# Kernel optimization log

Measured on AMD Instinct MI355X. Metric: run time of the kernel, lower is better.

Reference implementation:

```python
import jax, jax.numpy as jnp
import numpy as np

# config constants (match init_kwargs)
C = 1024
NH = 16
HS = C // NH
CHUNK = 64          # attn_chunk_size
TOPK = 32           # attn_topk
WINDOW = 4096       # kv_cache_window_size
MIN_KV = 16384      # min_kv_cache_size
MAX_KV = 32768      # max_kv_cache_size
SHORT = 4096        # short_sequence_criteria
CT = 65536          # incoming kv-cache length


def setup_inputs() -> dict:
    key = jax.random.key(0)
    ks = jax.random.split(key, 7)
    s = 1.0 / np.sqrt(C)
    return {
        "x": jax.random.normal(ks[0], (C,), jnp.float32),
        "k_cache": jax.random.normal(ks[1], (1, CT, C), jnp.float32),
        "v_cache": jax.random.normal(ks[2], (1, CT, C), jnp.float32),
        "Wr": jax.random.normal(ks[3], (C, C), jnp.float32) * s,
        "Wk": jax.random.normal(ks[4], (C, C), jnp.float32) * s,
        "Wv": jax.random.normal(ks[5], (C, C), jnp.float32) * s,
        "Wo": jax.random.normal(ks[6], (C, C), jnp.float32) * s,
    }


def _split_heads(t):  # (1, T, C) -> (1, NH, T, HS)
    return t.reshape(1, t.shape[1], NH, HS).transpose(0, 2, 1, 3)


def _update_kv_cache(q, k_cache, v_cache):
    # q: (1,1,C); caches: (1,CT,C). CT > MIN_KV so compression runs.
    past = CT - WINDOW
    kp = _split_heads(k_cache[:, :past])          # (1,NH,past,HS)
    vp = _split_heads(v_cache[:, :past])
    qh = _split_heads(q)                          # (1,NH,1,HS)
    scores = jnp.einsum("bhqd,bhkd->bhqk", qh, kp) / np.sqrt(HS)
    w = jax.nn.softmax(scores, axis=-1)           # (1,NH,1,past)
    vote = w.sum(axis=-2)                         # (1,NH,past)
    keep = MIN_KV - WINDOW                        # per-head tokens kept
    _, idx = jax.lax.top_k(vote, keep)            # (1,NH,keep), descending vote order
    kpc = jnp.take_along_axis(kp, idx[..., None], axis=2)  # (1,NH,keep,HS)
    vpc = jnp.take_along_axis(vp, idx[..., None], axis=2)
    kpc = kpc.transpose(0, 2, 1, 3).reshape(1, keep, C)
    vpc = vpc.transpose(0, 2, 1, 3).reshape(1, keep, C)
    k_new = jnp.concatenate([kpc, k_cache[:, past:]], axis=1)  # (1, MIN_KV, C)
    v_new = jnp.concatenate([vpc, v_cache[:, past:]], axis=1)
    return k_new, v_new


def reference(x, k_cache, v_cache, Wr, Wk, Wv, Wo):
    x2 = x[None, None, :]                         # (1,1,C)
    q = x2 @ Wr.T
    k = x2 @ Wk.T
    v = x2 @ Wv.T

    # CT > MAX_KV -> compress cache (eviction via attention vote per head)
    k_cache, v_cache = _update_kv_cache(q, k_cache, v_cache)
    CT2 = k_cache.shape[1]                        # MIN_KV = 16384 > SHORT -> sparse path

    num_chunks = CT2 // CHUNK
    kc = k_cache.reshape(1, num_chunks, CHUNK, C)
    vc = v_cache.reshape(1, num_chunks, CHUNK, C)
    chunk_key = kc.mean(axis=2)                   # (1,num_chunks,C)
    chunk_score = jnp.einsum("bqc,bkc->bqk", q, chunk_key)
    _, tidx = jax.lax.top_k(chunk_score[0, 0], TOPK)  # (TOPK,)
    topk_k = kc[:, tidx].reshape(1, TOPK * CHUNK, C)
    topk_v = vc[:, tidx].reshape(1, TOPK * CHUNK, C)

    k_comb = jnp.concatenate([topk_k, k], axis=1)  # (1, TOPK*CHUNK+1, C)
    v_comb = jnp.concatenate([topk_v, v], axis=1)

    qh = _split_heads(q)                          # (1,NH,1,HS)
    kh = _split_heads(k_comb)
    vh = _split_heads(v_comb)
    attn = jax.nn.softmax(
        jnp.einsum("bhqd,bhkd->bhqk", qh, kh) / np.sqrt(HS), axis=-1)
    y = jnp.einsum("bhqk,bhkd->bhqd", attn, vh)   # (1,NH,1,HS)
    y = y.transpose(0, 2, 1, 3).reshape(C)
    y = y @ Wo.T
    return y
```

## Files before the change

kernel.cpp:

```cpp
#include <hip/hip_runtime.h>
#include <stdint.h>

#define C      1024
#define NH     16
#define HS     64
#define CT     65536
#define PAST   61440
#define KEEP   12288
#define NCOMP  192
#define NSEL   32
#define NB     8192
#define NBLK   256

typedef unsigned long long ull;

#define LD_A(p)   __hip_atomic_load((p), __ATOMIC_RELAXED, __HIP_MEMORY_SCOPE_AGENT)
#define ST_A(p,v) __hip_atomic_store((p), (v), __ATOMIC_RELAXED, __HIP_MEMORY_SCOPE_AGENT)

__device__ __forceinline__ unsigned int desc_key(float f) {
    unsigned int b = __float_as_uint(f);
    return (b >> 31) ? b : (~b & 0x7FFFFFFFu);
}
__device__ __forceinline__ float u_to_f(unsigned int u) {
    unsigned int b = (u & 0x80000000u) ? u : (0x7FFFFFFFu - u);
    return __uint_as_float(b);
}
__device__ __forceinline__ int bin_of(float s, float hi, float scale) {
    int b = (int)((hi - s) * scale);
    return b < 0 ? 0 : (b > NB - 1 ? NB - 1 : b);
}
__device__ __forceinline__ void load_params(const unsigned* umin, const unsigned* umax,
                                            int h, float* hi, float* sc) {
    float h2 = u_to_f(umin[h]);
    float lo = u_to_f(umax[h]);
    float r = h2 - lo;
    *hi = h2;
    *sc = (r > 0.f) ? (float)(NB - 1) / r : 0.f;
}

#define GRPW 32
#define SITEW 288
__device__ __forceinline__ void gsync(unsigned* bar, int site) {
    __syncthreads();
    if (threadIdx.x == 0) {
        asm volatile("s_waitcnt vmcnt(0)" ::: "memory");
        unsigned* g    = bar + site * SITEW + (blockIdx.x >> 5) * GRPW;
        unsigned* root = bar + site * SITEW + 8 * GRPW;
        if (__hip_atomic_fetch_add(g, 1u, __ATOMIC_RELAXED, __HIP_MEMORY_SCOPE_AGENT) == 31u)
            __hip_atomic_fetch_add(root, 1u, __ATOMIC_RELAXED, __HIP_MEMORY_SCOPE_AGENT);
        while (LD_A(root) < 8u) __builtin_amdgcn_s_sleep(16);
    }
    __syncthreads();
}

__global__ void k_proj(const float* __restrict__ x, const float* __restrict__ Wr,
                       const float* __restrict__ Wk, const float* __restrict__ Wv,
                       float* __restrict__ q, float* __restrict__ kn, float* __restrict__ vn,
                       unsigned* __restrict__ hist, unsigned* __restrict__ umin,
                       unsigned* __restrict__ umax, ull* __restrict__ cs_fix,
                       unsigned* __restrict__ bar) {
    int id = blockIdx.x * 256 + threadIdx.x;
    if (id < NH * NB) hist[id] = 0;
    if (blockIdx.x >= 512 && blockIdx.x < 520)
        bar[(blockIdx.x - 512) * 256 + threadIdx.x] = 0u;
    if (blockIdx.x == 700) {
        if (threadIdx.x < 16) umin[threadIdx.x] = 0xFFFFFFFFu;
        else if (threadIdx.x < 32) umax[threadIdx.x - 16] = 0u;
    }
    if (blockIdx.x == 701 && threadIdx.x < 256) cs_fix[threadIdx.x] = 0ull;

    int w = blockIdx.x * (blockDim.x >> 6) + (threadIdx.x >> 6);
    int lane = threadIdx.x & 63;
    int mat = w >> 10, row = w & 1023;
    const float* W = (mat == 0) ? Wr : (mat == 1) ? Wk : Wv;
    const float4* Wrow = (const float4*)(W + (size_t)row * C);
    const float4* x4 = (const float4*)x;
    float acc = 0.f;
#pragma unroll
    for (int i = 0; i < 4; ++i) {
        float4 a = Wrow[i * 64 + lane];
        float4 b = x4[i * 64 + lane];
        acc += a.x * b.x + a.y * b.y + a.z * b.z + a.w * b.w;
    }
#pragma unroll
    for (int off = 32; off; off >>= 1) acc += __shfl_xor(acc, off);
    if (lane == 0) { (mat == 0 ? q : (mat == 1 ? kn : vn))[row] = acc; }
}

__global__ void k_scores(const float* __restrict__ kc, const float* __restrict__ q,
                         float* __restrict__ s, unsigned* __restrict__ umin,
                         unsigned* __restrict__ umax) {
    __shared__ float sc_l[4][16][17];
    __shared__ float smn[4][16], smx[4][16];
    int wave = threadIdx.x >> 6, lane = threadIdx.x & 63;
    int wid = blockIdx.x * 4 + wave;
    int t0 = wid * 16;
    const float4* q4 = (const float4*)q;
    float4 qv[4];
#pragma unroll
    for (int i = 0; i < 4; ++i) qv[i] = q4[i * 64 + lane];
    float mnv[4] = {3.4e38f, 3.4e38f, 3.4e38f, 3.4e38f};
    float mxv[4] = {-3.4e38f, -3.4e38f, -3.4e38f, -3.4e38f};
    for (int tt = 0; tt < 16; ++tt) {
        const float4* row = (const float4*)(kc + (size_t)(t0 + tt) * C);
        float acc[4];
#pragma unroll
        for (int i = 0; i < 4; ++i) {
            float4 a = row[i * 64 + lane];
            acc[i] = a.x * qv[i].x + a.y * qv[i].y + a.z * qv[i].z + a.w * qv[i].w;
        }
#pragma unroll
        for (int off = 8; off; off >>= 1) {
#pragma unroll
            for (int i = 0; i < 4; ++i) acc[i] += __shfl_xor(acc[i], off);
        }
        if ((lane & 15) == 0) {
            int g = lane >> 4;
#pragma unroll
            for (int i = 0; i < 4; ++i) {
                sc_l[wave][4 * i + g][tt] = acc[i];
                mnv[i] = fminf(mnv[i], acc[i]);
                mxv[i] = fmaxf(mxv[i], acc[i]);
            }
        }
    }
    __syncthreads();
    int tt2 = lane & 15;
#pragma unroll
    for (int r = 0; r < 4; ++r) {
        int h = r * 4 + (lane >> 4);
        s[(size_t)h * CT + t0 + tt2] = sc_l[wave][h][tt2];
    }
    if (blockIdx.x < 960) {
        if ((lane & 15) == 0) {
            int g = lane >> 4;
#pragma unroll
            for (int i = 0; i < 4; ++i) { smn[wave][4 * i + g] = mnv[i]; smx[wave][4 * i + g] = mxv[i]; }
        }
        __syncthreads();
        if (threadIdx.x < 16) {
            int h = threadIdx.x;
            float mn = smn[0][h], mx = smx[0][h];
            for (int w2 = 1; w2 < 4; ++w2) {
                mn = fminf(mn, smn[w2][h]);
                mx = fmaxf(mx, smx[w2][h]);
            }
            atomicMin(&umin[h], desc_key(mx));
            atomicMax(&umax[h], desc_key(mn));
        }
    }
}

__global__ __launch_bounds__(1024, 2) void k_mega(
        const float* __restrict__ s, const float* __restrict__ vc,
        const unsigned* __restrict__ umin, const unsigned* __restrict__ umax,
        unsigned* __restrict__ base, unsigned* __restrict__ Tarr,
        ull* __restrict__ G, unsigned* __restrict__ stok,
        ull* __restrict__ cs_fix, float* __restrict__ part,
        const float* __restrict__ q, const float* __restrict__ kn,
        const float* __restrict__ vn, const float* __restrict__ Wo,
        float* __restrict__ out, unsigned* __restrict__ bar) {
    const int bid = blockIdx.x, tid = threadIdx.x;
    const int lane = tid & 63, wave = tid >> 6;
    __shared__ __align__(16) char smem[40960];
    __shared__ unsigned tarr_l[16];
    __shared__ unsigned shT, shN;

    {
        unsigned* lh = (unsigned*)smem;
        int h = bid >> 4, seg = bid & 15;
        for (int i = tid; i < NB; i += 1024) lh[i] = 0;
        __syncthreads();
        float hi, sc; load_params(umin, umax, h, &hi, &sc);
        const float* sh = s + (size_t)h * CT + seg * 3840;
        for (int i = tid; i < 3840; i += 1024)
            atomicAdd(&lh[bin_of(sh[i], hi, sc)], 1u);
        __syncthreads();
        unsigned* gh = base + h * NB;
        for (int i = tid; i < NB; i += 1024) {
            unsigned c = lh[i];
            if (c) atomicAdd(&gh[i], c);
        }
    }
    gsync(bar, 0);

    if (bid < 16) {
        unsigned* wsum = (unsigned*)smem;
        unsigned* B = base + bid * NB;
        unsigned cnt[8];
        unsigned loc = 0;
        int b0 = tid * 8;
#pragma unroll
        for (int k = 0; k < 8; ++k) { cnt[k] = LD_A(&B[b0 + k]); loc += cnt[k]; }
        unsigned run = loc;
#pragma unroll
        for (int off = 1; off < 64; off <<= 1) {
            unsigned n = __shfl_up(run, off);
            if (lane >= off) run += n;
        }
        if (lane == 63) wsum[wave] = run;
        __syncthreads();
        if (wave == 0 && lane < 16) {
            unsigned v = wsum[lane];
#pragma unroll
            for (int off = 1; off < 16; off <<= 1) {
                unsigned n = __shfl_up(v, off);
                if (lane >= off) v += n;
            }
            wsum[lane] = v;
        }
        __syncthreads();
        unsigned r = run - loc + (wave ? wsum[wave - 1] : 0u);
#pragma unroll
        for (int k = 0; k < 8; ++k) {
            unsigned c = cnt[k];
            ST_A(&B[b0 + k], r);
            unsigned inc = r + c;
            if (r < KEEP && inc >= KEEP) ST_A(&Tarr[bid], (unsigned)(b0 + k));
            r = inc;
        }
    } else {
        int gw = (bid - 16) * 16 + wave;
        if (gw < NH * 64) {
            int h = gw >> 6, c2 = gw & 63;
            float v = s[(size_t)h * CT + PAST + c2 * 64 + lane];
            long long f = llrintf(v * 16777216.f);
#pragma unroll
            for (int off = 32; off; off >>= 1) f += __shfl_xor(f, off);
            if (lane == 0) atomicAdd(&cs_fix[NCOMP + c2], (ull)f);
        }
    }
    gsync(bar, 1);

    if (tid < 16) tarr_l[tid] = LD_A(&Tarr[tid]);
    __syncthreads();
    for (int i = bid * 1024 + tid; i < NH * PAST; i += NBLK * 1024) {
        int h = i / PAST, t = i - h * PAST;
        float hi, sc; load_params(umin, umax, h, &hi, &sc);
        float v = s[(size_t)h * CT + t];
        int b = bin_of(v, hi, sc);
        if ((unsigned)b <= tarr_l[h]) {
            unsigned pos = atomicAdd(&base[h * NB + b], 1u);
            ST_A(&G[(size_t)h * 65536 + pos], ((ull)desc_key(v) << 16) | (unsigned)t);
        }
    }
    gsync(bar, 2);

    {
        ull* csl = (ull*)smem;
        if (tid < NCOMP) csl[tid] = 0ull;
        int h = bid >> 4, seg = bid & 15;
        if (tid == 0) {
            unsigned T = LD_A(&Tarr[h]);
            shT = T;
            shN = LD_A(&base[h * NB + T]);
        }
        __syncthreads();
        float hi, sc; load_params(umin, umax, h, &hi, &sc);
        unsigned ncand = shN;
        const ull* Gh = G + (size_t)h * 65536;
        for (unsigned p = seg * 1024 + tid; p < ncand; p += 16384) {
            ull pk = Gh[p];
            unsigned u = (unsigned)(pk >> 16);
            float v = u_to_f(u);
            int b = bin_of(v, hi, sc);
            unsigned start = b ? LD_A(&base[h * NB + b - 1]) : 0u;
            unsigned end = LD_A(&base[h * NB + b]);
            unsigned rank = start;
            for (unsigned j = start; j < end; ++j) rank += (Gh[j] < pk) ? 1u : 0u;
            if (rank < KEEP) {
                ST_A(&stok[h * KEEP + rank], (unsigned)(pk & 0xFFFFull));
                long long f = llrintf(v * 16777216.f);
                atomicAdd(&csl[rank >> 6], (ull)f);
            }
        }
        __syncthreads();
        if (tid < NCOMP) {
            ull c = csl[tid];
            if (c) atomicAdd(&cs_fix[tid], c);
        }
    }
    gsync(bar, 3);

    {
        ull* key = (ull*)smem;
        unsigned* sel_l = (unsigned*)(smem + 2048);
        float* scm = (float*)(smem + 2176);
        float* exb = (float*)(smem + 2688);
        float* vbuf = (float*)(smem + 3200);
        if (tid < 256) {
            long long v = (long long)cs_fix[tid];
            ull bb = (ull)(v + (1ll << 45));
            key[tid] = (((1ull << 46) - bb) << 8) | (unsigned)tid;
        }
        __syncthreads();
        for (unsigned k = 2; k <= 256; k <<= 1) {
            for (unsigned j = k >> 1; j > 0; j >>= 1) {
                if (tid < 256) {
                    unsigned ixj = tid ^ j;
                    if (ixj > (unsigned)tid) {
                        ull a = key[tid], b = key[ixj];
                        bool up = ((tid & k) == 0);
                        if (up ? (a > b) : (a < b)) { key[tid] = b; key[ixj] = a; }
                    }
                }
                __syncthreads();
            }
        }
        if (tid < NSEL) sel_l[tid] = (unsigned)(key[tid] & 0xFFull);
        __syncthreads();

        int su = tid >> 9, sid = tid & 511;
        int p = bid * 2 + su;
        int h = p >> 5, ci = p & 31;
        int c = (int)sel_l[ci];
        int g = sid >> 3, q8 = sid & 7;
        int t = (c < NCOMP) ? (int)stok[h * KEEP + c * 64 + g]
                            : (PAST + (c - NCOMP) * 64 + g);
        if (q8 == 0) scm[su * 64 + g] = s[(size_t)h * CT + t] * 0.125f;
        __syncthreads();
        float m = -1e30f;
        for (int j = 0; j < 64; ++j) m = fmaxf(m, scm[su * 64 + j]);
        float e = expf(scm[su * 64 + g] - m);
        if (q8 == 0) exb[su * 64 + g] = e;
        const float4* vrow = (const float4*)(vc + (size_t)t * C + h * HS);
        float4 v0 = vrow[q8 * 2], v1 = vrow[q8 * 2 + 1];
        float* vb = vbuf + su * 4352 + g * 68 + q8 * 8;
        vb[0] = e * v0.x; vb[1] = e * v0.y; vb[2] = e * v0.z; vb[3] = e * v0.w;
        vb[4] = e * v1.x; vb[5] = e * v1.y; vb[6] = e * v1.z; vb[7] = e * v1.w;
        __syncthreads();
        if (sid < 64) {
            float acc = 0.f;
            for (int g2 = 0; g2 < 64; ++g2) acc += vbuf[su * 4352 + g2 * 68 + sid];
            float* P = part + (size_t)(h * 32 + ci) * 68;
            ST_A(&P[2 + sid], acc);
            if (sid == 0) {
                float es = 0.f;
                for (int g2 = 0; g2 < 64; ++g2) es += exb[su * 64 + g2];
                ST_A(&P[0], m);
                ST_A(&P[1], es);
            }
        }
    }
    gsync(bar, 4);
    if (bid >= 64) return;

    {
        float* yl = (float*)smem;
        float* qdl = (float*)(smem + 4096);
        if (tid < 16) {
            float qd = 0.f;
            for (int l = 0; l < 64; ++l) qd += q[tid * 64 + l] * kn[tid * 64 + l];
            qdl[tid] = qd;
        }
        __syncthreads();
        {
            int h = tid >> 6, ln = tid & 63;
            float a_new = qdl[h] * 0.125f;
            const float* P0 = part + (size_t)h * 32 * 68;
            float m = a_new;
            for (int ci = 0; ci < 32; ++ci) m = fmaxf(m, P0[ci * 68]);
            float den = expf(a_new - m);
            float acc = den * vn[h * HS + ln];
            for (int ci = 0; ci < 32; ++ci) {
                float w = expf(P0[ci * 68] - m);
                den += w * P0[ci * 68 + 1];
                acc += w * P0[ci * 68 + 2 + ln];
            }
            yl[tid] = acc / den;
        }
        __syncthreads();
        int r = bid * 16 + wave;
        const float4* Wrow = (const float4*)(Wo + (size_t)r * C);
        const float4* y4 = (const float4*)yl;
        float acc = 0.f;
#pragma unroll
        for (int i = 0; i < 4; ++i) {
            float4 a = Wrow[i * 64 + lane];
            float4 b = y4[i * 64 + lane];
            acc += a.x * b.x + a.y * b.y + a.z * b.z + a.w * b.w;
        }
#pragma unroll
        for (int off = 32; off; off >>= 1) acc += __shfl_xor(acc, off);
        if (lane == 0) out[r] = acc;
    }
}

extern "C" void kernel_launch(void* const* d_in, const int* in_sizes, int n_in,
                              void* d_out, int out_size, void* d_ws, size_t ws_size,
                              hipStream_t stream) {
    const float* x  = (const float*)d_in[0];
    const float* kc = (const float*)d_in[1];
    const float* vc = (const float*)d_in[2];
    const float* Wr = (const float*)d_in[3];
    const float* Wk = (const float*)d_in[4];
    const float* Wv = (const float*)d_in[5];
    const float* Wo = (const float*)d_in[6];
    float* out = (float*)d_out;
    char* ws = (char*)d_ws;

    float* q    = (float*)(ws + 0);
    float* kn   = (float*)(ws + 8192);
    float* vn   = (float*)(ws + 16384);
    ull* cs_fix = (ull*)(ws + 32768);
    float* part = (float*)(ws + 49152);
    unsigned* stok = (unsigned*)(ws + 196608);
    unsigned* umin = (unsigned*)(ws + 1048576);
    unsigned* umax = (unsigned*)(ws + 1048640);
    unsigned* Tarr = (unsigned*)(ws + 1048704);
    unsigned* bar  = (unsigned*)(ws + 1048832);
    unsigned* base = (unsigned*)(ws + 1114112);
    float* s = (float*)(ws + 2097152);
    ull* G = (ull*)(ws + 6291456);

    k_proj<<<768, 256, 0, stream>>>(x, Wr, Wk, Wv, q, kn, vn, base, umin, umax, cs_fix, bar);
    k_scores<<<1024, 256, 0, stream>>>(kc, q, s, umin, umax);
    k_mega<<<NBLK, 1024, 0, stream>>>(s, vc, umin, umax, base, Tarr, G, stok, cs_fix,
                                      part, q, kn, vn, Wo, out, bar);
}
```

Measured before the change: 143.4 us.

## Replace grid-wide barriers with per-head barriers and local histogram scans

Histogram building, prefix scan, and candidate scatter now happen per head among that head's 16 blocks, synchronised by a per-head counter barrier instead of three grid-wide barriers. Each block redoes the head's prefix scan in shared memory, and scatters from its own segment using a separate count array. The window-chunk fixed-point sum moves into k_scores' otherwise idle tail blocks. The aim is to cut global barrier latency and serial phases at the cost of redundant scans and more workspace zeroing.

Result: faster. 130.4 us (-9.0%).

```diff
diff --git a/kernel.cpp b/kernel.cpp
--- a/kernel.cpp
+++ b/kernel.cpp
@@ -38,29 +38,37 @@
     *sc = (r > 0.f) ? (float)(NB - 1) / r : 0.f;
 }
 
-#define GRPW 32
-#define SITEW 288
 __device__ __forceinline__ void gsync(unsigned* bar, int site) {
     __syncthreads();
     if (threadIdx.x == 0) {
         asm volatile("s_waitcnt vmcnt(0)" ::: "memory");
-        unsigned* g    = bar + site * SITEW + (blockIdx.x >> 5) * GRPW;
-        unsigned* root = bar + site * SITEW + 8 * GRPW;
+        unsigned* g    = bar + site * 288 + (blockIdx.x >> 5) * 32;
+        unsigned* root = bar + site * 288 + 256;
         if (__hip_atomic_fetch_add(g, 1u, __ATOMIC_RELAXED, __HIP_MEMORY_SCOPE_AGENT) == 31u)
             __hip_atomic_fetch_add(root, 1u, __ATOMIC_RELAXED, __HIP_MEMORY_SCOPE_AGENT);
         while (LD_A(root) < 8u) __builtin_amdgcn_s_sleep(16);
     }
     __syncthreads();
 }
+__device__ __forceinline__ void hsync(unsigned* bar, int site, int h) {
+    __syncthreads();
+    if (threadIdx.x == 0) {
+        asm volatile("s_waitcnt vmcnt(0)" ::: "memory");
+        unsigned* c = bar + 576 + (site * 16 + h) * 32;
+        __hip_atomic_fetch_add(c, 1u, __ATOMIC_RELAXED, __HIP_MEMORY_SCOPE_AGENT);
+        while (LD_A(c) < 16u) __builtin_amdgcn_s_sleep(8);
+    }
+    __syncthreads();
+}
 
 __global__ void k_proj(const float* __restrict__ x, const float* __restrict__ Wr,
                        const float* __restrict__ Wk, const float* __restrict__ Wv,
                        float* __restrict__ q, float* __restrict__ kn, float* __restrict__ vn,
-                       unsigned* __restrict__ hist, unsigned* __restrict__ umin,
+                       unsigned* __restrict__ hc, unsigned* __restrict__ umin,
                        unsigned* __restrict__ umax, ull* __restrict__ cs_fix,
                        unsigned* __restrict__ bar) {
-    int id = blockIdx.x * 256 + threadIdx.x;
-    if (id < NH * NB) hist[id] = 0;
+    int gid = blockIdx.x * 256 + threadIdx.x;
+    for (int i = gid; i < 2 * NH * NB; i += 196608) hc[i] = 0;
     if (blockIdx.x >= 512 && blockIdx.x < 520)
         bar[(blockIdx.x - 512) * 256 + threadIdx.x] = 0u;
     if (blockIdx.x == 700) {
@@ -89,9 +97,10 @@
 
 __global__ void k_scores(const float* __restrict__ kc, const float* __restrict__ q,
                          float* __restrict__ s, unsigned* __restrict__ umin,
-                         unsigned* __restrict__ umax) {
+                         unsigned* __restrict__ umax, ull* __restrict__ cs_fix) {
     __shared__ float sc_l[4][16][17];
     __shared__ float smn[4][16], smx[4][16];
+    __shared__ long long wred[4];
     int wave = threadIdx.x >> 6, lane = threadIdx.x & 63;
     int wid = blockIdx.x * 4 + wave;
     int t0 = wid * 16;
@@ -148,13 +157,25 @@
             atomicMin(&umin[h], desc_key(mx));
             atomicMax(&umax[h], desc_key(mn));
         }
+    } else {
+        int hh = threadIdx.x >> 4, tt = threadIdx.x & 15;
+        long long f = 0;
+#pragma unroll
+        for (int w2 = 0; w2 < 4; ++w2) f += llrintf(sc_l[w2][hh][tt] * 16777216.f);
+#pragma unroll
+        for (int off = 32; off; off >>= 1) f += __shfl_xor(f, off);
+        if (lane == 0) wred[wave] = f;
+        __syncthreads();
+        if (threadIdx.x == 0)
+            cs_fix[NCOMP + (blockIdx.x - 960)] =
+                (ull)(wred[0] + wred[1] + wred[2] + wred[3]);
     }
 }
 
 __global__ __launch_bounds__(1024, 2) void k_mega(
         const float* __restrict__ s, const float* __restrict__ vc,
         const unsigned* __restrict__ umin, const unsigned* __restrict__ umax,
-        unsigned* __restrict__ base, unsigned* __restrict__ Tarr,
+        unsigned* __restrict__ hist, unsigned* __restrict__ cnt,
         ull* __restrict__ G, unsigned* __restrict__ stok,
         ull* __restrict__ cs_fix, float* __restrict__ part,
         const float* __restrict__ q, const float* __restrict__ kn,
@@ -162,36 +183,34 @@
         float* __restrict__ out, unsigned* __restrict__ bar) {
     const int bid = blockIdx.x, tid = threadIdx.x;
     const int lane = tid & 63, wave = tid >> 6;
+    const int h = bid >> 4, seg = bid & 15;
     __shared__ __align__(16) char smem[40960];
-    __shared__ unsigned tarr_l[16];
     __shared__ unsigned shT, shN;
-
-    {
-        unsigned* lh = (unsigned*)smem;
-        int h = bid >> 4, seg = bid & 15;
+    __shared__ unsigned wsum[16];
+
+    float hi, sc; load_params(umin, umax, h, &hi, &sc);
+    unsigned* lh = (unsigned*)smem;
+
+    {
         for (int i = tid; i < NB; i += 1024) lh[i] = 0;
         __syncthreads();
-        float hi, sc; load_params(umin, umax, h, &hi, &sc);
         const float* sh = s + (size_t)h * CT + seg * 3840;
         for (int i = tid; i < 3840; i += 1024)
             atomicAdd(&lh[bin_of(sh[i], hi, sc)], 1u);
         __syncthreads();
-        unsigned* gh = base + h * NB;
+        unsigned* gh = hist + h * NB;
         for (int i = tid; i < NB; i += 1024) {
             unsigned c = lh[i];
             if (c) atomicAdd(&gh[i], c);
         }
     }
-    gsync(bar, 0);
-
-    if (bid < 16) {
-        unsigned* wsum = (unsigned*)smem;
-        unsigned* B = base + bid * NB;
-        unsigned cnt[8];
-        unsigned loc = 0;
-        int b0 = tid * 8;
-#pragma unroll
-        for (int k = 0; k < 8; ++k) { cnt[k] = LD_A(&B[b0 + k]); loc += cnt[k]; }
+    hsync(bar, 0, h);
+
+    {
+        const unsigned* gh = hist + h * NB;
+        unsigned c8[8]; unsigned loc = 0; int b0 = tid * 8;
+#pragma unroll
+        for (int k = 0; k < 8; ++k) { c8[k] = gh[b0 + k]; loc += c8[k]; }
         unsigned run = loc;
 #pragma unroll
         for (int off = 1; off < 64; off <<= 1) {
@@ -213,59 +232,43 @@
         unsigned r = run - loc + (wave ? wsum[wave - 1] : 0u);
 #pragma unroll
         for (int k = 0; k < 8; ++k) {
-            unsigned c = cnt[k];
-            ST_A(&B[b0 + k], r);
+            unsigned c = c8[k];
+            lh[b0 + k] = r;
             unsigned inc = r + c;
-            if (r < KEEP && inc >= KEEP) ST_A(&Tarr[bid], (unsigned)(b0 + k));
+            if (r < KEEP && inc >= KEEP) { shT = (unsigned)(b0 + k); shN = inc; }
             r = inc;
         }
-    } else {
-        int gw = (bid - 16) * 16 + wave;
-        if (gw < NH * 64) {
-            int h = gw >> 6, c2 = gw & 63;
-            float v = s[(size_t)h * CT + PAST + c2 * 64 + lane];
-            long long f = llrintf(v * 16777216.f);
-#pragma unroll
-            for (int off = 32; off; off >>= 1) f += __shfl_xor(f, off);
-            if (lane == 0) atomicAdd(&cs_fix[NCOMP + c2], (ull)f);
-        }
-    }
-    gsync(bar, 1);
-
-    if (tid < 16) tarr_l[tid] = LD_A(&Tarr[tid]);
-    __syncthreads();
-    for (int i = bid * 1024 + tid; i < NH * PAST; i += NBLK * 1024) {
-        int h = i / PAST, t = i - h * PAST;
-        float hi, sc; load_params(umin, umax, h, &hi, &sc);
-        float v = s[(size_t)h * CT + t];
-        int b = bin_of(v, hi, sc);
-        if ((unsigned)b <= tarr_l[h]) {
-            unsigned pos = atomicAdd(&base[h * NB + b], 1u);
-            ST_A(&G[(size_t)h * 65536 + pos], ((ull)desc_key(v) << 16) | (unsigned)t);
-        }
-    }
-    gsync(bar, 2);
-
-    {
-        ull* csl = (ull*)smem;
+    }
+    __syncthreads();
+    const unsigned T = shT, ncand = shN;
+
+    {
+        const float* sh = s + (size_t)h * CT + seg * 3840;
+        unsigned* ch = cnt + h * NB;
+        ull* Gh = G + (size_t)h * 65536;
+        for (int i = tid; i < 3840; i += 1024) {
+            float v = sh[i];
+            int b = bin_of(v, hi, sc);
+            if ((unsigned)b <= T) {
+                unsigned pos = lh[b] + atomicAdd(&ch[b], 1u);
+                ST_A(&Gh[pos], ((ull)desc_key(v) << 16) | (unsigned)(seg * 3840 + i));
+            }
+        }
+    }
+    hsync(bar, 1, h);
+
+    {
+        ull* csl = (ull*)(smem + 32768);
         if (tid < NCOMP) csl[tid] = 0ull;
-        int h = bid >> 4, seg = bid & 15;
-        if (tid == 0) {
-            unsigned T = LD_A(&Tarr[h]);
-            shT = T;
-            shN = LD_A(&base[h * NB + T]);
-        }
-        __syncthreads();
-        float hi, sc; load_params(umin, umax, h, &hi, &sc);
-        unsigned ncand = shN;
+        __syncthreads();
         const ull* Gh = G + (size_t)h * 65536;
         for (unsigned p = seg * 1024 + tid; p < ncand; p += 16384) {
             ull pk = Gh[p];
             unsigned u = (unsigned)(pk >> 16);
             float v = u_to_f(u);
             int b = bin_of(v, hi, sc);
-            unsigned start = b ? LD_A(&base[h * NB + b - 1]) : 0u;
-            unsigned end = LD_A(&base[h * NB + b]);
+            unsigned start = lh[b];
+            unsigned end = (b == NB - 1) ? ncand : lh[b + 1];
             unsigned rank = start;
             for (unsigned j = start; j < end; ++j) rank += (Gh[j] < pk) ? 1u : 0u;
             if (rank < KEEP) {
@@ -280,7 +283,7 @@
             if (c) atomicAdd(&cs_fix[tid], c);
         }
     }
-    gsync(bar, 3);
+    gsync(bar, 0);
 
     {
         ull* key = (ull*)smem;
@@ -312,18 +315,18 @@
 
         int su = tid >> 9, sid = tid & 511;
         int p = bid * 2 + su;
-        int h = p >> 5, ci = p & 31;
+        int hh = p >> 5, ci = p & 31;
         int c = (int)sel_l[ci];
         int g = sid >> 3, q8 = sid & 7;
-        int t = (c < NCOMP) ? (int)stok[h * KEEP + c * 64 + g]
+        int t = (c < NCOMP) ? (int)stok[hh * KEEP + c * 64 + g]
                             : (PAST + (c - NCOMP) * 64 + g);
-        if (q8 == 0) scm[su * 64 + g] = s[(size_t)h * CT + t] * 0.125f;
+        if (q8 == 0) scm[su * 64 + g] = s[(size_t)hh * CT + t] * 0.125f;
         __syncthreads();
         float m = -1e30f;
         for (int j = 0; j < 64; ++j) m = fmaxf(m, scm[su * 64 + j]);
         float e = expf(scm[su * 64 + g] - m);
         if (q8 == 0) exb[su * 64 + g] = e;
-        const float4* vrow = (const float4*)(vc + (size_t)t * C + h * HS);
+        const float4* vrow = (const float4*)(vc + (size_t)t * C + hh * HS);
         float4 v0 = vrow[q8 * 2], v1 = vrow[q8 * 2 + 1];
         float* vb = vbuf + su * 4352 + g * 68 + q8 * 8;
         vb[0] = e * v0.x; vb[1] = e * v0.y; vb[2] = e * v0.z; vb[3] = e * v0.w;
@@ -332,7 +335,7 @@
         if (sid < 64) {
             float acc = 0.f;
             for (int g2 = 0; g2 < 64; ++g2) acc += vbuf[su * 4352 + g2 * 68 + sid];
-            float* P = part + (size_t)(h * 32 + ci) * 68;
+            float* P = part + (size_t)(hh * 32 + ci) * 68;
             ST_A(&P[2 + sid], acc);
             if (sid == 0) {
                 float es = 0.f;
@@ -342,7 +345,7 @@
             }
         }
     }
-    gsync(bar, 4);
+    gsync(bar, 1);
     if (bid >= 64) return;
 
     {
@@ -355,13 +358,13 @@
         }
         __syncthreads();
         {
-            int h = tid >> 6, ln = tid & 63;
-            float a_new = qdl[h] * 0.125f;
-            const float* P0 = part + (size_t)h * 32 * 68;
+            int hh = tid >> 6, ln = tid & 63;
+            float a_new = qdl[hh] * 0.125f;
+            const float* P0 = part + (size_t)hh * 32 * 68;
             float m = a_new;
             for (int ci = 0; ci < 32; ++ci) m = fmaxf(m, P0[ci * 68]);
             float den = expf(a_new - m);
-            float acc = den * vn[h * HS + ln];
+            float acc = den * vn[hh * HS + ln];
             for (int ci = 0; ci < 32; ++ci) {
                 float w = expf(P0[ci * 68] - m);
                 den += w * P0[ci * 68 + 1];
@@ -407,14 +410,14 @@
     unsigned* stok = (unsigned*)(ws + 196608);
     unsigned* umin = (unsigned*)(ws + 1048576);
     unsigned* umax = (unsigned*)(ws + 1048640);
-    unsigned* Tarr = (unsigned*)(ws + 1048704);
     unsigned* bar  = (unsigned*)(ws + 1048832);
-    unsigned* base = (unsigned*)(ws + 1114112);
-    float* s = (float*)(ws + 2097152);
-    ull* G = (ull*)(ws + 6291456);
-
-    k_proj<<<768, 256, 0, stream>>>(x, Wr, Wk, Wv, q, kn, vn, base, umin, umax, cs_fix, bar);
-    k_scores<<<1024, 256, 0, stream>>>(kc, q, s, umin, umax);
-    k_mega<<<NBLK, 1024, 0, stream>>>(s, vc, umin, umax, base, Tarr, G, stok, cs_fix,
+    unsigned* hist = (unsigned*)(ws + 1114112);
+    unsigned* cnt  = (unsigned*)(ws + 1638400);
+    float* s = (float*)(ws + 2621440);
+    ull* G = (ull*)(ws + 7340032);
+
+    k_proj<<<768, 256, 0, stream>>>(x, Wr, Wk, Wv, q, kn, vn, hist, umin, umax, cs_fix, bar);
+    k_scores<<<1024, 256, 0, stream>>>(kc, q, s, umin, umax, cs_fix);
+    k_mega<<<NBLK, 1024, 0, stream>>>(s, vc, umin, umax, hist, cnt, G, stok, cs_fix,
                                       part, q, kn, vn, Wo, out, bar);
 }
```
